# Optimization experiments

Hardware: AMD Instinct MI355X
Metric: run time of the kernel (lower is better)

## Reference

```python
import jax, jax.numpy as jnp
import numpy as np
from jax import lax

T, C_IN, H0, W0 = 15, 6, 160, 160
C1, C2 = 128, 256
K1, K2 = 5, 2
THR1, THR2 = 10.0, 1.0
KWTA, RAD = 8, 1
W_MEAN, W_STD = 0.8, 0.05


def setup_inputs() -> dict:
    key = jax.random.key(0)
    k1, k2, k3 = jax.random.split(key, 3)
    # cumulative binary spike wave: each input neuron fires at a random time (or never)
    t_fire = jax.random.randint(k1, (C_IN, H0, W0), 0, 2 * T)
    inp = (jnp.arange(T)[:, None, None, None] >= t_fire[None]).astype(jnp.float32)
    w1 = W_MEAN + W_STD * jax.random.normal(k2, (C1, C_IN, K1, K1), jnp.float32)
    w2 = W_MEAN + W_STD * jax.random.normal(k3, (C2, C1, K2, K2), jnp.float32)
    return {"inp": inp, "w1": w1, "w2": w2, "layer_idx": 2}


def _conv(x, w):
    # x: [T, C, H, W] (time acts as batch), VALID conv, no bias (SpykeTorch snn.Convolution)
    return lax.conv_general_dilated(x, w, (1, 1), 'VALID',
                                    dimension_numbers=('NCHW', 'OIHW', 'NCHW'))


def _pad(x, p):
    return jnp.pad(x, ((0, 0), (0, 0), (p, p), (p, p)))


def _pool(x):
    # sf.pooling(s, 2, 2, 1): max-pool kernel 2, stride 2, padding 1 per time step
    return lax.reduce_window(x, -jnp.inf, lax.max,
                             (1, 1, 2, 2), (1, 1, 2, 2),
                             ((0, 0), (0, 0), (1, 1), (1, 1)))


def _fire(v, thr):
    # sf.fire with return_thresholded_potentials=True: zero out sub-threshold potentials
    v = jnp.where(v < thr, 0.0, v)
    return jnp.sign(v), v


def _pointwise_inhibition(v):
    # v: [T, C, H, W] nonneg.  At each spatial position, the feature with the max
    t, c = v.shape[0], v.shape[1]
    max_vals = v.max(axis=1)                      # [T,H,W]
    max_idx = v.argmax(axis=1).astype(jnp.int32)  # [T,H,W] winner channel per time
    clamp = jnp.sign(max_vals)                    # [T,H,W] any-spike indicator
    earliest = jnp.clip(t - clamp.sum(axis=0).astype(jnp.int32), 0, t - 1)  # [H,W]
    winner = jnp.take_along_axis(max_idx, earliest[None], axis=0)[0]        # [H,W]
    alive = clamp[-1]                             # [H,W] 1 if any spike ever
    coef = (jnp.arange(c)[:, None, None] == winner[None]).astype(v.dtype) * alive
    return v * coef[None]


def _get_k_winners(v, s, kwta, rad):
    # Greedy k-WTA with per-feature and spatial (radius) inhibition (NMS-like).
    t, c, h, w = v.shape
    earliest = jnp.clip(t - s.sum(axis=0).astype(jnp.int32), 0, t - 1)  # [C,H,W]
    vals = jnp.take_along_axis(v, earliest[None], axis=0)[0]            # potential at first spike
    trunc = s * vals
    big = trunc.max() * t                                               # earlier-spike dominance term
    trunc = trunc + s * big
    total = trunc.sum(axis=0)                                           # [C,H,W]

    ch_ids = jnp.arange(c)
    row_ids = jnp.arange(h)
    col_ids = jnp.arange(w)

    def step(total, _):
        idx = jnp.argmax(total.reshape(-1))
        mv = total.reshape(-1)[idx]
        f = (idx // (h * w)).astype(jnp.int32)
        rem = idx % (h * w)
        r = (rem // w).astype(jnp.int32)
        col = (rem % w).astype(jnp.int32)
        active = mv != 0
        kill = ((ch_ids == f)[:, None, None]
                | ((jnp.abs(row_ids - r) <= rad)[:, None]
                   & (jnp.abs(col_ids - col) <= rad)[None, :])[None])
        new_total = jnp.where(active, jnp.where(kill, 0.0, total), total)
        winner = jnp.where(active, jnp.stack([f, r, col]), -1)
        return new_total, winner

    _, winners = lax.scan(step, total, None, length=kwta)
    return winners  # [kwta, 3] (feature,row,col), -1 rows = inactive


def reference(inp, w1, w2, layer_idx):
    # training path, layer_idx == 2 (deepest branch)
    x = _pad(inp, 2)                       # [T,6,164,164]
    v = _conv(x, w1)                       # [T,128,160,160]
    s, v = _fire(v, THR1)
    s_in = _pad(_pool(s), 1)               # [T,128,83,83]
    s_in = _pointwise_inhibition(s_in)
    v = _conv(s_in, w2)                    # [T,256,82,82]
    s, v = _fire(v, THR2)
    v = _pointwise_inhibition(v)
    s = jnp.sign(v)
    winners = _get_k_winners(v, s, KWTA, RAD)
    return s, v, winners
```

## Files before the change

kernel.cpp:

```cpp
#include <hip/hip_runtime.h>

#define T_ 15
#define CIN 6
#define H0 160
#define W0 160
#define C1_ 128
#define C2_ 256
#define HP 83
#define H2 82
#define NPIX (H0*W0)
#define NIN (CIN*NPIX)
#define NPOS (H2*H2)
#define NS (T_*C2_*NPOS)
#define THR1 10.0f
#define THR2 1.0f
#define NF1 2048
#define NF2 2048

__global__ __launch_bounds__(256) void k_mega(const float* __restrict__ inp,
                                              const float* __restrict__ w1,
                                              const float* __restrict__ w2,
                                              unsigned int* __restrict__ maskg,
                                              float* __restrict__ w1T,
                                              float* __restrict__ w2T,
                                              unsigned int* __restrict__ bigbits,
                                              uint4* __restrict__ fill_dst,
                                              size_t nA, int nf) {
    __shared__ unsigned char tft[CIN * 20 * 20];
    __shared__ int cnt[16 * 256];
    int b = blockIdx.x;
    int tid = threadIdx.x;

    if (b < 100) {
        int ty0 = (b / 10) * 16, tx0 = (b % 10) * 16;
        for (int i = tid; i < CIN * 400; i += 256) {
            int ci = i / 400, rem = i % 400;
            int ly = rem / 20, lx = rem % 20;
            int y = ty0 + ly - 2, x = tx0 + lx - 2;
            unsigned char tv = 15;
            if ((unsigned)y < (unsigned)H0 && (unsigned)x < (unsigned)W0) {
                float c = 0.f;
                int base = ci * NPIX + y * W0 + x;
#pragma unroll
                for (int t = 0; t < T_; t++) c += inp[(size_t)t * NIN + base];
                tv = (unsigned char)(15 - (int)(c + 0.5f));
            }
            tft[i] = tv;
        }
        __syncthreads();

        int tyl = tid >> 4, txl = tid & 15;
        int pix = (ty0 + tyl) * W0 + (tx0 + txl);
        int* col = cnt + tid;

#pragma unroll
        for (int w = 0; w < 5; w++) {
            int j0 = w * 32, j1 = (w == 4) ? 150 : (j0 + 32);
#pragma unroll
            for (int q = 0; q < 16; q++) col[q * 256] = 0;
#pragma unroll 32
            for (int j = j0; j < j1; j++) {
                int ci = j / 25, r = j % 25, ky = r / 5, kx = r % 5;
                int tfv = tft[ci * 400 + (tyl + ky) * 20 + (txl + kx)];
                col[tfv * 256] |= 1u << (j & 31);
            }
#pragma unroll
            for (int t = 0; t < 15; t++)
                maskg[(size_t)(t * 5 + w) * NPIX + pix] = (unsigned)col[t * 256];
        }
    } else if (b < 175) {
        if (b == 100 && tid == 0) *bigbits = 0u;
        int idx = (b - 100) * 256 + tid;
        int j = idx >> 7, c = idx & 127;
        w1T[idx] = w1[c * 150 + j];
    } else if (b < 687) {
        int idx = (b - 175) * 256 + tid;
        int o = idx & 255, kcc = idx >> 8;
        int cc = kcc & 127, k = kcc >> 7;
        w2T[idx] = w2[o * 512 + cc * 4 + k];
    } else {
        size_t stride = (size_t)nf * 256;
        uint4 z = make_uint4(0u, 0u, 0u, 0u);
        for (size_t i = (size_t)(b - 687) * 256 + tid; i < nA; i += stride)
            fill_dst[i] = z;
    }
}

__global__ __launch_bounds__(256) void k1_main(const unsigned int* __restrict__ maskg,
                                               const float* __restrict__ w1T,
                                               unsigned char* __restrict__ fst1,
                                               uint4* __restrict__ fill_dst,
                                               size_t nA, size_t n16, int nf) {
    int b = blockIdx.x;
    int tid = threadIdx.x;
    if (b >= 6400) {
        size_t stride = (size_t)nf * 256;
        uint4 z = make_uint4(0u, 0u, 0u, 0u);
        for (size_t i = nA + (size_t)(b - 6400) * 256 + tid; i < n16; i += stride)
            fill_dst[i] = z;
        return;
    }
    int pix = b * 4 + (tid >> 6);
    int lane = tid & 63;
    const float* wb = w1T + 2 * lane;

    float v0 = 0.f, v1 = 0.f;
    int f0 = 15, f1 = 15;
    for (int t = 0; t < 15; ++t) {
        float b0 = 0.f, b1 = 0.f;
#pragma unroll
        for (int w = 0; w < 5; ++w) {
            unsigned int m = maskg[(size_t)(t * 5 + w) * NPIX + pix];
            int base = w * 32;
            while (m) {
                int j = base + __builtin_ctz(m);
                m &= m - 1;
                float2 ww = *(const float2*)(wb + j * C1_);
                b0 += ww.x; b1 += ww.y;
            }
        }
        v0 += b0; v1 += b1;
        f0 = (f0 == 15 && v0 >= THR1) ? t : f0;
        f1 = (f1 == 15 && v1 >= THR1) ? t : f1;
        if (__all((f0 < 15) & (f1 < 15))) break;
    }
    *(uchar2*)(fst1 + (size_t)pix * C1_ + 2 * lane) =
        make_uchar2((unsigned char)f0, (unsigned char)f1);
}

__global__ __launch_bounds__(256) void k2_pool(const unsigned char* __restrict__ fst1,
                                               unsigned char* __restrict__ win_t,
                                               unsigned char* __restrict__ win_ch) {
    int pos = blockIdx.x * 4 + (threadIdx.x >> 6);
    int lane = threadIdx.x & 63;
    if (pos >= HP * HP) return;
    int py = pos / HP, px = pos % HP;
    if (py == 0 || py == HP - 1 || px == 0 || px == HP - 1) {
        if (lane == 0) { win_t[pos] = 15; win_ch[pos] = 0; }
        return;
    }
    int y0 = 2 * py - 3, x0 = 2 * px - 3;
    int m0 = 15, m1 = 15;
#pragma unroll
    for (int dy = 0; dy < 2; dy++) {
        int y = y0 + dy;
        if ((unsigned)y < (unsigned)H0) {
#pragma unroll
            for (int dx = 0; dx < 2; dx++) {
                int x = x0 + dx;
                if ((unsigned)x < (unsigned)W0) {
                    uchar2 f = *(const uchar2*)(fst1 + (size_t)(y * W0 + x) * C1_ + 2 * lane);
                    m0 = f.x < m0 ? f.x : m0;
                    m1 = f.y < m1 ? f.y : m1;
                }
            }
        }
    }
    int k0 = (m0 << 8) | (2 * lane);
    int k1 = (m1 << 8) | (2 * lane + 1);
    int key = k0 < k1 ? k0 : k1;
#pragma unroll
    for (int off = 32; off > 0; off >>= 1) {
        int other = __shfl_xor(key, off);
        key = other < key ? other : key;
    }
    if (lane == 0) {
        win_t[pos] = (unsigned char)(key >> 8);
        win_ch[pos] = (unsigned char)(key & 255);
    }
}

__global__ __launch_bounds__(256) void kz_fill(uint4* __restrict__ dst, size_t n16,
                                               unsigned int* __restrict__ bigbits) {
    size_t stride = (size_t)gridDim.x * 256;
    uint4 z = make_uint4(0u, 0u, 0u, 0u);
    for (size_t i = (size_t)blockIdx.x * 256 + threadIdx.x; i < n16; i += stride)
        dst[i] = z;
    if (blockIdx.x == 0 && threadIdx.x == 0) *bigbits = 0u;
}

__global__ __launch_bounds__(256) void k3_conv2(const unsigned char* __restrict__ win_t,
                                                const unsigned char* __restrict__ win_ch,
                                                const float* __restrict__ w2T,
                                                float* __restrict__ s_out,
                                                float* __restrict__ v_out,
                                                float* __restrict__ vals,
                                                int* __restrict__ nsp_arr,
                                                int* __restrict__ ow_arr,
                                                unsigned int* __restrict__ bigbits) {
    int p = blockIdx.x * 4 + (threadIdx.x >> 6);
    int lane = threadIdx.x & 63;
    int y2 = p / H2, x2 = p % H2;

    int tj[4]; int ccv[4];
#pragma unroll
    for (int k = 0; k < 4; k++) {
        int dy = k >> 1, dx = k & 1;
        int pi = (y2 + dy) * HP + (x2 + dx);
        tj[k] = win_t[pi];
        ccv[k] = win_ch[pi];
    }

    float wq[4][4];
    unsigned int mq[4];
    unsigned int lane_or = 0u;
#pragma unroll
    for (int q = 0; q < 4; q++) {
        int ch = q * 64 + lane;
#pragma unroll
        for (int k = 0; k < 4; k++)
            wq[q][k] = (tj[k] < 15) ? w2T[(k * C1_ + ccv[k]) * 256 + ch] : 0.0f;
        unsigned int m = 0u;
#pragma unroll
        for (int t = 0; t < T_; t++) {
            float v = 0.f;
#pragma unroll
            for (int k = 0; k < 4; k++) v += (t >= tj[k]) ? wq[q][k] : 0.f;
            m |= (v >= THR2) ? (1u << t) : 0u;
        }
        mq[q] = m;
        lane_or |= m;
    }

#pragma unroll
    for (int off = 32; off > 0; off >>= 1) lane_or |= __shfl_xor(lane_or, off);
    unsigned int om = lane_or;
    int count = __popc(om & 0x7FFFu);
    int earliest = 15 - count;
    earliest = earliest < 0 ? 0 : (earliest > 14 ? 14 : earliest);
    int alive = (om >> 14) & 1;

    unsigned long long best = 0ull;
    float bw0 = 0.f, bw1 = 0.f, bw2 = 0.f, bw3 = 0.f;
    unsigned int bm = 0u;
#pragma unroll
    for (int q = 0; q < 4; q++) {
        int ch = q * 64 + lane;
        float v = 0.f;
#pragma unroll
        for (int k = 0; k < 4; k++) v += (earliest >= tj[k]) ? wq[q][k] : 0.f;
        float zval = (v < THR2) ? 0.f : v;
        unsigned long long key =
            ((unsigned long long)__float_as_uint(zval) << 16) |
            (unsigned long long)(1023 - ch);
        if (key > best) {
            best = key;
            bw0 = wq[q][0]; bw1 = wq[q][1]; bw2 = wq[q][2]; bw3 = wq[q][3];
            bm = mq[q];
        }
    }
    unsigned long long gbest = best;
#pragma unroll
    for (int off = 32; off > 0; off >>= 1) {
        unsigned long long other = __shfl_xor(gbest, off);
        gbest = other > gbest ? other : gbest;
    }

    if (alive) {
        int wo = 1023 - (int)(gbest & 0xFFFFull);
        if ((wo & 63) == lane && best == gbest) {
            int nsp = __popc(bm & 0x7FFFu);
            int e2 = 15 - nsp;
            e2 = e2 < 0 ? 0 : (e2 > 14 ? 14 : e2);
            float vv = 0.f;
#pragma unroll
            for (int k = 0; k < 4; k++) {
                float wk = (k == 0) ? bw0 : (k == 1) ? bw1 : (k == 2) ? bw2 : bw3;
                vv += (e2 >= tj[k]) ? wk : 0.f;
            }
            vv = (vv < THR2) ? 0.f : vv;
            vals[p] = vv; nsp_arr[p] = nsp; ow_arr[p] = wo;
            if (nsp > 0) atomicMax(bigbits, __float_as_uint(vv));
#pragma unroll
            for (int t = 0; t < T_; t++) {
                if ((bm >> t) & 1u) {
                    float vt = 0.f;
                    vt += (t >= tj[0]) ? bw0 : 0.f;
                    vt += (t >= tj[1]) ? bw1 : 0.f;
                    vt += (t >= tj[2]) ? bw2 : 0.f;
                    vt += (t >= tj[3]) ? bw3 : 0.f;
                    int idx = ((t * C2_ + wo) * H2 + y2) * H2 + x2;
                    v_out[idx] = vt;
                    s_out[idx] = 1.0f;
                }
            }
        }
    } else if (lane == 0) {
        vals[p] = 0.f; nsp_arr[p] = 0; ow_arr[p] = 0;
    }
}

__global__ __launch_bounds__(1024) void k4_kwta(const float* __restrict__ vals,
                                                const int* __restrict__ nsp,
                                                const int* __restrict__ ow,
                                                const unsigned int* __restrict__ bigbits,
                                                float* __restrict__ wout) {
    __shared__ float tot[NPOS];
    __shared__ short och[NPOS];
    __shared__ unsigned long long amax;
    int tid = threadIdx.x;
    float big = __uint_as_float(*bigbits) * 15.0f;

    for (int p = tid; p < NPOS; p += 1024) {
        int n = nsp[p];
        tot[p] = (n > 0) ? (float)n * (vals[p] + big) : 0.0f;
        och[p] = (short)ow[p];
    }
    if (tid == 0) amax = 0ull;
    __syncthreads();

    for (int it = 0; it < 8; it++) {
        unsigned long long best = 0ull;
        for (int p = tid; p < NPOS; p += 1024) {
            float tv = tot[p];
            if (tv > 0.0f) {
                unsigned int k = (unsigned)och[p] * (unsigned)NPOS + (unsigned)p;
                unsigned long long pk =
                    ((unsigned long long)__float_as_uint(tv) << 21) |
                    (unsigned long long)(0x1FFFFFu - k);
                best = pk > best ? pk : best;
            }
        }
#pragma unroll
        for (int off = 32; off > 0; off >>= 1) {
            unsigned long long other = __shfl_xor(best, off);
            best = other > best ? other : best;
        }
        if ((tid & 63) == 0) atomicMax(&amax, best);
        __syncthreads();
        unsigned long long mx = amax;
        __syncthreads();
        if (tid == 0) amax = 0ull;

        if (mx == 0ull) {
            if (tid == 0) {
                wout[it * 3 + 0] = -1.f; wout[it * 3 + 1] = -1.f; wout[it * 3 + 2] = -1.f;
            }
        } else {
            unsigned int k = 0x1FFFFFu - (unsigned)(mx & 0x1FFFFFull);
            int f = (int)(k / NPOS), pp = (int)(k % NPOS);
            int r = pp / H2, col = pp % H2;
            if (tid == 0) {
                wout[it * 3 + 0] = (float)f; wout[it * 3 + 1] = (float)r; wout[it * 3 + 2] = (float)col;
            }
            for (int p = tid; p < NPOS; p += 1024) {
                int pr = p / H2, pc = p % H2;
                bool kill = (och[p] == (short)f) ||
                            (pr >= r - 1 && pr <= r + 1 && pc >= col - 1 && pc <= col + 1);
                if (kill) tot[p] = 0.0f;
            }
        }
        __syncthreads();
    }
}

extern "C" void kernel_launch(void* const* d_in, const int* in_sizes, int n_in,
                              void* d_out, int out_size, void* d_ws, size_t ws_size,
                              hipStream_t stream) {
    const float* inp = (const float*)d_in[0];
    const float* w1  = (const float*)d_in[1];
    const float* w2  = (const float*)d_in[2];

    float* out = (float*)d_out;
    float* s_out = out;
    float* v_out = out + (size_t)NS;
    float* wnr   = out + 2 * (size_t)NS;

    size_t need = (size_t)15 << 20;
    bool big_ws = ws_size >= need;
    char* scratch = big_ws ? (char*)d_ws
                           : (char*)d_out + (size_t)NS * sizeof(float);
    unsigned int* maskg = (unsigned int*)scratch;
    unsigned char* fst1 = (unsigned char*)(scratch + (8 << 20));
    float* w1T = (float*)(scratch + (12 << 20));
    float* w2T = (float*)(scratch + (13 << 20));
    char* smol = big_ws ? (char*)d_ws + (14 << 20) : (char*)d_ws;
    unsigned char* win_t  = (unsigned char*)smol;
    unsigned char* win_ch = (unsigned char*)smol + 8192;
    float* vals = (float*)(smol + 16384);
    int*   nsp  = (int*)(smol + 49152);
    int*   ow   = (int*)(smol + 81920);
    unsigned int* bigbits = (unsigned int*)(smol + 114688);

    size_t n16 = (size_t)out_size / 4;
    size_t nA  = big_ws ? n16 / 2 : 0;
    int nf1 = big_ws ? NF1 : 0;
    int nf2 = big_ws ? NF2 : 0;

    hipLaunchKernelGGL(k_mega, dim3(687 + nf1), dim3(256), 0, stream,
                       inp, w1, w2, maskg, w1T, w2T, bigbits, (uint4*)d_out, nA, nf1);
    hipLaunchKernelGGL(k1_main, dim3(6400 + nf2), dim3(256), 0, stream,
                       maskg, w1T, fst1, (uint4*)d_out, nA, n16, nf2);
    hipLaunchKernelGGL(k2_pool, dim3((HP * HP + 3) / 4), dim3(256), 0, stream,
                       fst1, win_t, win_ch);
    if (!big_ws)
        hipLaunchKernelGGL(kz_fill, dim3(4096), dim3(256), 0, stream,
                           (uint4*)d_out, n16, bigbits);
    hipLaunchKernelGGL(k3_conv2, dim3(NPOS / 4), dim3(256), 0, stream,
                       win_t, win_ch, w2T, s_out, v_out, vals, nsp, ow, bigbits);
    hipLaunchKernelGGL(k4_kwta, dim3(1), dim3(1024), 0, stream, vals, nsp, ow, bigbits, wnr);
}
```

Before: 199.6 us.

## Fuse first four kernels into one cooperative persistent kernel with grid syncs

```diff
diff --git a/kernel.cpp b/kernel.cpp
--- a/kernel.cpp
+++ b/kernel.cpp
@@ -1,4 +1,7 @@
 #include <hip/hip_runtime.h>
+#include <hip/hip_cooperative_groups.h>
+
+namespace cg = cooperative_groups;
 
 #define T_ 15
 #define CIN 6
@@ -17,6 +20,247 @@
 #define NF1 2048
 #define NF2 2048
 
+__global__ __launch_bounds__(256, 4) void k_coop(
+    const float* __restrict__ inp, const float* __restrict__ w1,
+    const float* __restrict__ w2, unsigned int* __restrict__ maskg,
+    float* __restrict__ w1T, float* __restrict__ w2T,
+    unsigned char* __restrict__ fst1, unsigned char* __restrict__ win_t,
+    unsigned char* __restrict__ win_ch, float* __restrict__ vals,
+    int* __restrict__ nsp_arr, int* __restrict__ ow_arr,
+    unsigned int* __restrict__ bigbits, float* __restrict__ s_out,
+    float* __restrict__ v_out, uint4* __restrict__ fill_dst, size_t n16) {
+    __shared__ unsigned char tft[CIN * 20 * 20];
+    __shared__ int cnt[16 * 256];
+    cg::grid_group gg = cg::this_grid();
+    int b = blockIdx.x, tid = threadIdx.x;
+    int nb = gridDim.x;
+    int nwaves = nb * 4;
+    int wid = b * 4 + (tid >> 6);
+    int lane = tid & 63;
+    const uint4 z4 = make_uint4(0u, 0u, 0u, 0u);
+    size_t nA = n16 / 2;
+
+    for (int u = b; u < 687; u += nb) {
+        if (u < 100) {
+            __syncthreads();
+            int ty0 = (u / 10) * 16, tx0 = (u % 10) * 16;
+            for (int i = tid; i < CIN * 400; i += 256) {
+                int ci = i / 400, rem = i % 400;
+                int ly = rem / 20, lx = rem % 20;
+                int y = ty0 + ly - 2, x = tx0 + lx - 2;
+                unsigned char tv = 15;
+                if ((unsigned)y < (unsigned)H0 && (unsigned)x < (unsigned)W0) {
+                    float c = 0.f;
+                    int base = ci * NPIX + y * W0 + x;
+#pragma unroll
+                    for (int t = 0; t < T_; t++) c += inp[(size_t)t * NIN + base];
+                    tv = (unsigned char)(15 - (int)(c + 0.5f));
+                }
+                tft[i] = tv;
+            }
+            __syncthreads();
+            int tyl = tid >> 4, txl = tid & 15;
+            int pix = (ty0 + tyl) * W0 + (tx0 + txl);
+            int* col = cnt + tid;
+#pragma unroll
+            for (int w = 0; w < 5; w++) {
+                int j0 = w * 32, j1 = (w == 4) ? 150 : (j0 + 32);
+#pragma unroll
+                for (int q = 0; q < 16; q++) col[q * 256] = 0;
+#pragma unroll 32
+                for (int j = j0; j < j1; j++) {
+                    int ci = j / 25, r = j % 25, ky = r / 5, kx = r % 5;
+                    int tfv = tft[ci * 400 + (tyl + ky) * 20 + (txl + kx)];
+                    col[tfv * 256] |= 1u << (j & 31);
+                }
+#pragma unroll
+                for (int t = 0; t < 15; t++)
+                    maskg[(size_t)(t * 5 + w) * NPIX + pix] = (unsigned)col[t * 256];
+            }
+        } else if (u < 175) {
+            int idx = (u - 100) * 256 + tid;
+            int j = idx >> 7, c = idx & 127;
+            w1T[idx] = w1[c * 150 + j];
+        } else {
+            int idx = (u - 175) * 256 + tid;
+            int o = idx & 255, kcc = idx >> 8;
+            int cc = kcc & 127, k = kcc >> 7;
+            w2T[idx] = w2[o * 512 + cc * 4 + k];
+        }
+    }
+    if (b == 0 && tid == 0) *bigbits = 0u;
+    for (size_t i = (size_t)b * 256 + tid; i < nA; i += (size_t)nb * 256)
+        fill_dst[i] = z4;
+    gg.sync();
+
+    {
+        const float* wb = w1T + 2 * lane;
+        for (int pix = wid; pix < NPIX; pix += nwaves) {
+            float v0 = 0.f, v1 = 0.f;
+            int f0 = 15, f1 = 15;
+            for (int t = 0; t < 15; ++t) {
+                float b0 = 0.f, b1 = 0.f;
+#pragma unroll
+                for (int w = 0; w < 5; ++w) {
+                    unsigned int m = maskg[(size_t)(t * 5 + w) * NPIX + pix];
+                    int base = w * 32;
+                    while (m) {
+                        int j = base + __builtin_ctz(m);
+                        m &= m - 1;
+                        float2 ww = *(const float2*)(wb + j * C1_);
+                        b0 += ww.x; b1 += ww.y;
+                    }
+                }
+                v0 += b0; v1 += b1;
+                f0 = (f0 == 15 && v0 >= THR1) ? t : f0;
+                f1 = (f1 == 15 && v1 >= THR1) ? t : f1;
+                if (__all((f0 < 15) & (f1 < 15))) break;
+            }
+            *(uchar2*)(fst1 + (size_t)pix * C1_ + 2 * lane) =
+                make_uchar2((unsigned char)f0, (unsigned char)f1);
+        }
+    }
+    for (size_t i = nA + (size_t)b * 256 + tid; i < n16; i += (size_t)nb * 256)
+        fill_dst[i] = z4;
+    gg.sync();
+
+    for (int pos = wid; pos < HP * HP; pos += nwaves) {
+        int py = pos / HP, px = pos % HP;
+        if (py == 0 || py == HP - 1 || px == 0 || px == HP - 1) {
+            if (lane == 0) { win_t[pos] = 15; win_ch[pos] = 0; }
+            continue;
+        }
+        int y0 = 2 * py - 3, x0 = 2 * px - 3;
+        int m0 = 15, m1 = 15;
+#pragma unroll
+        for (int dy = 0; dy < 2; dy++) {
+            int y = y0 + dy;
+            if ((unsigned)y < (unsigned)H0) {
+#pragma unroll
+                for (int dx = 0; dx < 2; dx++) {
+                    int x = x0 + dx;
+                    if ((unsigned)x < (unsigned)W0) {
+                        uchar2 f = *(const uchar2*)(fst1 + (size_t)(y * W0 + x) * C1_ + 2 * lane);
+                        m0 = f.x < m0 ? f.x : m0;
+                        m1 = f.y < m1 ? f.y : m1;
+                    }
+                }
+            }
+        }
+        int k0 = (m0 << 8) | (2 * lane);
+        int k1 = (m1 << 8) | (2 * lane + 1);
+        int key = k0 < k1 ? k0 : k1;
+#pragma unroll
+        for (int off = 32; off > 0; off >>= 1) {
+            int other = __shfl_xor(key, off);
+            key = other < key ? other : key;
+        }
+        if (lane == 0) {
+            win_t[pos] = (unsigned char)(key >> 8);
+            win_ch[pos] = (unsigned char)(key & 255);
+        }
+    }
+    gg.sync();
+
+    for (int p = wid; p < NPOS; p += nwaves) {
+        int y2 = p / H2, x2 = p % H2;
+        int tj[4]; int ccv[4];
+#pragma unroll
+        for (int k = 0; k < 4; k++) {
+            int dy = k >> 1, dx = k & 1;
+            int pi = (y2 + dy) * HP + (x2 + dx);
+            tj[k] = win_t[pi];
+            ccv[k] = win_ch[pi];
+        }
+        float wq[4][4];
+        unsigned int mq[4];
+        unsigned int lane_or = 0u;
+#pragma unroll
+        for (int q = 0; q < 4; q++) {
+            int ch = q * 64 + lane;
+#pragma unroll
+            for (int k = 0; k < 4; k++)
+                wq[q][k] = (tj[k] < 15) ? w2T[(k * C1_ + ccv[k]) * 256 + ch] : 0.0f;
+            unsigned int m = 0u;
+#pragma unroll
+            for (int t = 0; t < T_; t++) {
+                float v = 0.f;
+#pragma unroll
+                for (int k = 0; k < 4; k++) v += (t >= tj[k]) ? wq[q][k] : 0.f;
+                m |= (v >= THR2) ? (1u << t) : 0u;
+            }
+            mq[q] = m;
+            lane_or |= m;
+        }
+#pragma unroll
+        for (int off = 32; off > 0; off >>= 1) lane_or |= __shfl_xor(lane_or, off);
+        unsigned int om = lane_or;
+        int count = __popc(om & 0x7FFFu);
+        int earliest = 15 - count;
+        earliest = earliest < 0 ? 0 : (earliest > 14 ? 14 : earliest);
+        int alive = (om >> 14) & 1;
+
+        unsigned long long best = 0ull;
+        float bw0 = 0.f, bw1 = 0.f, bw2 = 0.f, bw3 = 0.f;
+        unsigned int bm = 0u;
+#pragma unroll
+        for (int q = 0; q < 4; q++) {
+            int ch = q * 64 + lane;
+            float v = 0.f;
+#pragma unroll
+            for (int k = 0; k < 4; k++) v += (earliest >= tj[k]) ? wq[q][k] : 0.f;
+            float zval = (v < THR2) ? 0.f : v;
+            unsigned long long key =
+                ((unsigned long long)__float_as_uint(zval) << 16) |
+                (unsigned long long)(1023 - ch);
+            if (key > best) {
+                best = key;
+                bw0 = wq[q][0]; bw1 = wq[q][1]; bw2 = wq[q][2]; bw3 = wq[q][3];
+                bm = mq[q];
+            }
+        }
+        unsigned long long gbest = best;
+#pragma unroll
+        for (int off = 32; off > 0; off >>= 1) {
+            unsigned long long other = __shfl_xor(gbest, off);
+            gbest = other > gbest ? other : gbest;
+        }
+
+        if (alive) {
+            int wo = 1023 - (int)(gbest & 0xFFFFull);
+            if ((wo & 63) == lane && best == gbest) {
+                int nsp = __popc(bm & 0x7FFFu);
+                int e2 = 15 - nsp;
+                e2 = e2 < 0 ? 0 : (e2 > 14 ? 14 : e2);
+                float vv = 0.f;
+#pragma unroll
+                for (int k = 0; k < 4; k++) {
+                    float wk = (k == 0) ? bw0 : (k == 1) ? bw1 : (k == 2) ? bw2 : bw3;
+                    vv += (e2 >= tj[k]) ? wk : 0.f;
+                }
+                vv = (vv < THR2) ? 0.f : vv;
+                vals[p] = vv; nsp_arr[p] = nsp; ow_arr[p] = wo;
+                if (nsp > 0) atomicMax(bigbits, __float_as_uint(vv));
+#pragma unroll
+                for (int t = 0; t < T_; t++) {
+                    if ((bm >> t) & 1u) {
+                        float vt = 0.f;
+                        vt += (t >= tj[0]) ? bw0 : 0.f;
+                        vt += (t >= tj[1]) ? bw1 : 0.f;
+                        vt += (t >= tj[2]) ? bw2 : 0.f;
+                        vt += (t >= tj[3]) ? bw3 : 0.f;
+                        int idx = ((t * C2_ + wo) * H2 + y2) * H2 + x2;
+                        v_out[idx] = vt;
+                        s_out[idx] = 1.0f;
+                    }
+                }
+            }
+        } else if (lane == 0) {
+            vals[p] = 0.f; nsp_arr[p] = 0; ow_arr[p] = 0;
+        }
+    }
+}
+
 __global__ __launch_bounds__(256) void k_mega(const float* __restrict__ inp,
                                               const float* __restrict__ w1,
                                               const float* __restrict__ w2,
@@ -52,7 +296,6 @@
         int tyl = tid >> 4, txl = tid & 15;
         int pix = (ty0 + tyl) * W0 + (tx0 + txl);
         int* col = cnt + tid;
-
 #pragma unroll
         for (int w = 0; w < 5; w++) {
             int j0 = w * 32, j1 = (w == 4) ? 150 : (j0 + 32);
@@ -383,20 +626,41 @@
     unsigned int* bigbits = (unsigned int*)(smol + 114688);
 
     size_t n16 = (size_t)out_size / 4;
-    size_t nA  = big_ws ? n16 / 2 : 0;
-    int nf1 = big_ws ? NF1 : 0;
-    int nf2 = big_ws ? NF2 : 0;
-
-    hipLaunchKernelGGL(k_mega, dim3(687 + nf1), dim3(256), 0, stream,
-                       inp, w1, w2, maskg, w1T, w2T, bigbits, (uint4*)d_out, nA, nf1);
-    hipLaunchKernelGGL(k1_main, dim3(6400 + nf2), dim3(256), 0, stream,
-                       maskg, w1T, fst1, (uint4*)d_out, nA, n16, nf2);
-    hipLaunchKernelGGL(k2_pool, dim3((HP * HP + 3) / 4), dim3(256), 0, stream,
-                       fst1, win_t, win_ch);
-    if (!big_ws)
-        hipLaunchKernelGGL(kz_fill, dim3(4096), dim3(256), 0, stream,
-                           (uint4*)d_out, n16, bigbits);
-    hipLaunchKernelGGL(k3_conv2, dim3(NPOS / 4), dim3(256), 0, stream,
-                       win_t, win_ch, w2T, s_out, v_out, vals, nsp, ow, bigbits);
+    uint4* fill_dst = (uint4*)d_out;
+
+    bool coop_done = false;
+    if (big_ws) {
+        int maxb = 0;
+        hipError_t qe = hipOccupancyMaxActiveBlocksPerMultiprocessor(&maxb, k_coop, 256, 0);
+        if (qe == hipSuccess && maxb >= 1) {
+            int grid = maxb * 256;
+            if (grid > 1024) grid = 1024;
+            void* args[] = {(void*)&inp, (void*)&w1, (void*)&w2, (void*)&maskg,
+                            (void*)&w1T, (void*)&w2T, (void*)&fst1, (void*)&win_t,
+                            (void*)&win_ch, (void*)&vals, (void*)&nsp, (void*)&ow,
+                            (void*)&bigbits, (void*)&s_out, (void*)&v_out,
+                            (void*)&fill_dst, (void*)&n16};
+            hipError_t le = hipLaunchCooperativeKernel(k_coop, dim3(grid), dim3(256),
+                                                       args, 0, stream);
+            coop_done = (le == hipSuccess);
+        }
+    }
+
+    if (!coop_done) {
+        size_t nA  = big_ws ? n16 / 2 : 0;
+        int nf1 = big_ws ? NF1 : 0;
+        int nf2 = big_ws ? NF2 : 0;
+        hipLaunchKernelGGL(k_mega, dim3(687 + nf1), dim3(256), 0, stream,
+                           inp, w1, w2, maskg, w1T, w2T, bigbits, fill_dst, nA, nf1);
+        hipLaunchKernelGGL(k1_main, dim3(6400 + nf2), dim3(256), 0, stream,
+                           maskg, w1T, fst1, fill_dst, nA, n16, nf2);
+        hipLaunchKernelGGL(k2_pool, dim3((HP * HP + 3) / 4), dim3(256), 0, stream,
+                           fst1, win_t, win_ch);
+        if (!big_ws)
+            hipLaunchKernelGGL(kz_fill, dim3(4096), dim3(256), 0, stream,
+                               fill_dst, n16, bigbits);
+        hipLaunchKernelGGL(k3_conv2, dim3(NPOS / 4), dim3(256), 0, stream,
+                           win_t, win_ch, w2T, s_out, v_out, vals, nsp, ow, bigbits);
+    }
     hipLaunchKernelGGL(k4_kwta, dim3(1), dim3(1024), 0, stream, vals, nsp, ow, bigbits, wnr);
 }
```

Result: slower. 475.4 us (+138.2%).
